# Kernel tuning notes

Measured on AMD Instinct MI355X. Metric: run time of the kernel, lower is better.

## Reference

```python
import jax, jax.numpy as jnp
import numpy as np

GROUP = 4
SG = 4          # shared_gp
C = 256         # inchannels
N = 1024
BS = 16         # GROUP * batch
EPS = 1e-6


def _ln(x, g, b):
    # torch LayerNorm over last dim, biased variance, eps=1e-6
    mu = jnp.mean(x, axis=-1, keepdims=True)
    var = jnp.var(x, axis=-1, keepdims=True)
    return (x - mu) / jnp.sqrt(var + EPS) * g + b


def setup_inputs() -> dict:
    key = jax.random.key(0)
    ks = jax.random.split(key, 12)
    cg = C // SG
    s_conv = 1.0 / np.sqrt(cg)
    s_full = 1.0 / np.sqrt(C)
    return {
        "x": jax.random.normal(ks[0], (BS, C, N), jnp.float32),
        # grouped 1x1 convs (bias=False): weight (SG, C/SG out, C/SG in)
        "Wq": jax.random.normal(ks[1], (SG, cg, cg), jnp.float32) * s_conv,
        "Wk": jax.random.normal(ks[2], (SG, cg, cg), jnp.float32) * s_conv,
        # v conv: full 1x1 conv with bias
        "Wv": jax.random.normal(ks[3], (C, C), jnp.float32) * s_full,
        "bv": jax.random.normal(ks[4], (C,), jnp.float32) * 0.01,
        "ln1_g": jnp.ones((C,), jnp.float32),
        "ln1_b": jnp.zeros((C,), jnp.float32),
        "W1": jax.random.normal(ks[5], (4 * C, C), jnp.float32) * s_full,
        "b1": jax.random.normal(ks[6], (4 * C,), jnp.float32) * 0.01,
        "W2": jax.random.normal(ks[7], (C, 4 * C), jnp.float32) * (1.0 / np.sqrt(4 * C)),
        "b2": jax.random.normal(ks[8], (C,), jnp.float32) * 0.01,
        "ln2_g": jnp.ones((C,), jnp.float32),
        "ln2_b": jnp.zeros((C,), jnp.float32),
    }


def reference(x, Wq, Wk, Wv, bv, ln1_g, ln1_b, W1, b1, W2, b2, ln2_g, ln2_b):
    bs, ch, n = x.shape
    group, sg = GROUP, SG
    b = bs // group
    cg = ch // sg
    first = x[:b]          # (b, C, N)
    last = x[b:]           # ((g-1)*b, C, N)

    # grouped 1x1 convs: y[.,g,o,n] = sum_i W[g,o,i] * x[.,g,i,n]
    xq = jnp.einsum('goi,Bgin->Bgon', Wq, last.reshape((group - 1) * b, sg, cg, n))
    xq = xq.reshape(group - 1, b, sg, cg, n)              # (g-1, b, sg, cg, N)
    xk = jnp.einsum('goi,bgin->bgon', Wk, first.reshape(b, sg, cg, n))  # (b, sg, cg, N)
    xv = jnp.einsum('oc,bcn->bon', Wv, first) + bv[None, :, None]        # (b, C, N)

    # energy: q^T k per shared group, summed over shared groups -> (g-1, b, N, N)
    energy = jnp.einsum('gbscn,bscm->gbnm', xq, xk)
    attn = jax.nn.softmax(energy, axis=-1)
    # x_r[g,b,c,m] = sum_n v[b,c,n] attn[g,b,n,m], scaled by 1/sqrt(C)
    x_r = jnp.einsum('bcn,gbnm->gbcm', xv, attn) / jnp.sqrt(jnp.float32(ch))

    # faithful to torch: vstack (group-major) then view(batch, group-1, ...).mean(1)
    x_r = x_r.reshape(b, group - 1, ch, n).mean(axis=1)   # (b, C, N)

    h = _ln((first + x_r).transpose(0, 2, 1), ln1_g, ln1_b)  # (b, N, C)
    h = h + jax.nn.relu(h @ W1.T + b1) @ W2.T + b2
    h = jax.nn.relu(_ln(h, ln2_g, ln2_b))
    out_first = h.transpose(0, 2, 1)                       # (b, C, N)
    return jnp.concatenate([out_first, last], axis=0)
```

## Files before the change

kernel.cpp:

```cpp
#include <hip/hip_runtime.h>

#define CC 256
#define NN 1024
#define CN (CC*NN)

typedef __attribute__((ext_vector_type(8))) short short8;
typedef __attribute__((ext_vector_type(8))) unsigned short u16x8;
typedef __attribute__((ext_vector_type(4))) float f32x4;

__device__ __forceinline__ unsigned short f2bf(float x) {
  unsigned u = __float_as_uint(x);
  u = u + 0x7fffu + ((u >> 16) & 1u);
  return (unsigned short)(u >> 16);
}
__device__ __forceinline__ float bf2f(unsigned short b) {
  return __uint_as_float(((unsigned)b) << 16);
}
__device__ __forceinline__ void gload_lds16(const unsigned short* g, unsigned short* l) {
  __builtin_amdgcn_global_load_lds(
      (const __attribute__((address_space(1))) unsigned short*)g,
      (__attribute__((address_space(3))) unsigned short*)l, 16, 0, 0);
}

__global__ __launch_bounds__(256) void prep_kernel(
    const float* __restrict__ x, const float* __restrict__ Wq,
    const float* __restrict__ Wk, const float4* __restrict__ Wv,
    const float4* __restrict__ W1, const float4* __restrict__ W2,
    unsigned short* __restrict__ wv_bf, unsigned short* __restrict__ w1_bf,
    unsigned short* __restrict__ w2_bf, unsigned short* __restrict__ xT,
    unsigned short* __restrict__ xqT, unsigned short* __restrict__ xkT) {
  __shared__ float shbuf[64 * 133];
  int bz = blockIdx.x, t = threadIdx.x;
  if (bz < 576) {
    int id = bz * 256 + t;
    const float4* s; unsigned short* d; int k;
    if (id < 16384)      { s = Wv; d = wv_bf; k = id; }
    else if (id < 81920) { s = W1; d = w1_bf; k = id - 16384; }
    else                 { s = W2; d = w2_bf; k = id - 81920; }
    float4 v = s[k];
    ushort4 o; o.x = f2bf(v.x); o.y = f2bf(v.y); o.z = f2bf(v.z); o.w = f2bf(v.w);
    *(ushort4*)&d[k * 4] = o;
  } else if (bz < 832) {
    float (*tile)[65] = (float(*)[65])shbuf;
    int zz = bz - 576;
    int b = zz >> 6, c0 = ((zz >> 4) & 3) * 64, n0 = (zz & 15) * 64;
    int tr = t >> 6, tc = t & 63;
#pragma unroll
    for (int r = 0; r < 16; ++r) {
      int c = tr + r * 4;
      tile[c][tc] = x[(long)b * CN + (long)(c0 + c) * NN + n0 + tc];
    }
    __syncthreads();
#pragma unroll
    for (int r = 0; r < 16; ++r) {
      int n = tr + r * 4;
      xT[(long)b * CN + (long)(n0 + n) * CC + c0 + tc] = f2bf(tile[tc][n]);
    }
  } else {
    float (*xs)[68] = (float(*)[68])shbuf;
    float (*Ws)[65] = (float(*)[65])(shbuf + 64 * 68);
    int zz = bz - 832;
    int z = zz >> 6, g = (zz >> 4) & 3, n0 = (zz & 15) * 64;
    const float* src; const float* W; unsigned short* dst;
    if (z < 12) { src = x + (long)(4 + z) * CN; W = Wq; dst = xqT + (long)z * CN; }
    else        { src = x + (long)(z - 12) * CN; W = Wk; dst = xkT + (long)(z - 12) * CN; }
    int tr = t >> 6, tc = t & 63;
#pragma unroll
    for (int r = 0; r < 16; ++r) {
      int i = tr + r * 4;
      xs[i][tc] = src[(long)(g * 64 + i) * NN + n0 + tc];
      Ws[i][tc] = W[(g * 64 + i) * 64 + tc];
    }
    __syncthreads();
    int o = tc, q = tr;
    float acc[16];
#pragma unroll
    for (int k = 0; k < 16; ++k) acc[k] = 0.f;
    for (int i = 0; i < 64; ++i) {
      float w = Ws[o][i];
      const float4* xr4 = (const float4*)&xs[i][q * 16];
#pragma unroll
      for (int k = 0; k < 4; ++k) {
        float4 v = xr4[k];
        acc[4*k+0] += w * v.x; acc[4*k+1] += w * v.y;
        acc[4*k+2] += w * v.z; acc[4*k+3] += w * v.w;
      }
    }
#pragma unroll
    for (int k = 0; k < 16; ++k)
      dst[(long)(n0 + q * 16 + k) * CC + g * 64 + o] = f2bf(acc[k]);
  }
}

template<int BIASROW, int BIASCOL, int RELU, int RES, int OUTBF, int STATS>
__global__ __launch_bounds__(256) void mgemm(
    const unsigned short* __restrict__ A, const unsigned short* __restrict__ B,
    void* __restrict__ Cout, const float* __restrict__ bias,
    const float* __restrict__ res, float2* __restrict__ part,
    int lda, int ldb, int ldc, int K,
    long sA, int amod, long sB, int bmod, long sC, long sR, float alpha) {
  __shared__ unsigned short As[128 * 32];
  __shared__ unsigned short Bs[128 * 32];
  int z = blockIdx.z;
  A += (long)(z % amod) * sA;
  B += (long)(z % bmod) * sB;
  int t = threadIdx.x, w = t >> 6, l = t & 63;
  int wr = w >> 1, wc = w & 1;
  long i0 = blockIdx.y * 128, j0 = blockIdx.x * 128;
  f32x4 acc[4][4];
#pragma unroll
  for (int a = 0; a < 4; ++a)
#pragma unroll
    for (int b = 0; b < 4; ++b) acc[a][b] = (f32x4){0.f, 0.f, 0.f, 0.f};
  int lr = l & 15, lk = (l >> 4) * 8;
  for (int k0 = 0; k0 < K; k0 += 32) {
#pragma unroll
    for (int it = 0; it < 2; ++it) {
      int chunk = t + it * 256;
      int row = chunk >> 2, kq = chunk & 3;
      gload_lds16(A + (i0 + row) * (long)lda + k0 + kq * 8, &As[chunk * 8]);
      gload_lds16(B + (j0 + row) * (long)ldb + k0 + kq * 8, &Bs[chunk * 8]);
    }
    __syncthreads();
    short8 af[4], bfr[4];
#pragma unroll
    for (int f = 0; f < 4; ++f) af[f]  = *(const short8*)&As[(wr * 64 + f * 16 + lr) * 32 + lk];
#pragma unroll
    for (int f = 0; f < 4; ++f) bfr[f] = *(const short8*)&Bs[(wc * 64 + f * 16 + lr) * 32 + lk];
#pragma unroll
    for (int fm = 0; fm < 4; ++fm)
#pragma unroll
      for (int fn = 0; fn < 4; ++fn)
        acc[fm][fn] = __builtin_amdgcn_mfma_f32_16x16x32_bf16(af[fm], bfr[fn], acc[fm][fn], 0, 0, 0);
    __syncthreads();
  }
  long cz = (long)z * sC;
  long rz = (long)z * sR;
  int li = (l >> 4) * 4, lj = l & 15;
#pragma unroll
  for (int fm = 0; fm < 4; ++fm)
#pragma unroll
    for (int fn = 0; fn < 4; ++fn) {
      long ib = i0 + wr * 64 + fm * 16 + li;
      long j  = j0 + wc * 64 + fn * 16 + lj;
#pragma unroll
      for (int r = 0; r < 4; ++r) {
        long i = ib + r;
        float v = acc[fm][fn][r] * alpha;
        if (BIASCOL) v += bias[j];
        if (BIASROW) v += bias[i];
        if (RES)     v += res[rz + i * ldc + j];
        if (RELU)    v = fmaxf(v, 0.f);
        if (OUTBF) ((unsigned short*)Cout)[cz + i * ldc + j] = f2bf(v);
        else       ((float*)Cout)[cz + i * ldc + j] = v;
      }
    }
  if (STATS) {
    int chunk = blockIdx.y * 2 + wr;
#pragma unroll
    for (int fn = 0; fn < 4; ++fn) {
      float mx = -1e30f;
#pragma unroll
      for (int fm = 0; fm < 4; ++fm)
#pragma unroll
        for (int r = 0; r < 4; ++r) mx = fmaxf(mx, acc[fm][fn][r]);
      mx = fmaxf(mx, __shfl_xor(mx, 16));
      mx = fmaxf(mx, __shfl_xor(mx, 32));
      float sm = 0.f;
#pragma unroll
      for (int fm = 0; fm < 4; ++fm)
#pragma unroll
        for (int r = 0; r < 4; ++r) sm += __expf(acc[fm][fn][r] - mx);
      sm += __shfl_xor(sm, 16);
      sm += __shfl_xor(sm, 32);
      if (l < 16) {
        long n = j0 + wc * 64 + fn * 16 + l;
        part[((long)z * 16 + chunk) * NN + n] = make_float2(mx, sm);
      }
    }
  }
}

__global__ __launch_bounds__(256) void pv_gemm(
    const unsigned short* __restrict__ E, const unsigned short* __restrict__ XV,
    const float2* __restrict__ part, float* __restrict__ xrp) {
  __shared__ unsigned short As[128 * 32];
  __shared__ unsigned short Bs[128 * 32];
  __shared__ float Ms[256];
  __shared__ float Ds[256];
  int z = blockIdx.z;
  int q = z >> 2, s = z & 3;
  const unsigned short* A = E + (long)q * NN * NN + s * 256;
  const unsigned short* B = XV + (long)(q & 3) * CN + s * 256;
  int t = threadIdx.x;
  {
    int n = s * 256 + t;
    float mx = -1e30f;
#pragma unroll
    for (int c = 0; c < 16; ++c) mx = fmaxf(mx, part[((long)q * 16 + c) * NN + n].x);
    float sm = 0.f;
#pragma unroll
    for (int c = 0; c < 16; ++c) {
      float2 p = part[((long)q * 16 + c) * NN + n];
      sm += p.y * __expf(p.x - mx);
    }
    Ms[t] = mx;
    Ds[t] = 1.f / sm;
  }
  int w = t >> 6, l = t & 63;
  int wr = w >> 1, wc = w & 1;
  long i0 = blockIdx.y * 128, j0 = blockIdx.x * 128;
  f32x4 acc[4][4];
#pragma unroll
  for (int a = 0; a < 4; ++a)
#pragma unroll
    for (int b = 0; b < 4; ++b) acc[a][b] = (f32x4){0.f, 0.f, 0.f, 0.f};
  int lr = l & 15, lk = (l >> 4) * 8;
  int ar = t >> 1, ah = (t & 1) * 16;
  __syncthreads();
  for (int k0 = 0; k0 < 256; k0 += 32) {
#pragma unroll
    for (int it = 0; it < 2; ++it) {
      int chunk = t + it * 256;
      int row = chunk >> 2, kq = chunk & 3;
      gload_lds16(B + (j0 + row) * 1024L + k0 + kq * 8, &Bs[chunk * 8]);
    }
    u16x8 e0 = *(const u16x8*)&A[(i0 + ar) * 1024L + k0 + ah];
    u16x8 e1 = *(const u16x8*)&A[(i0 + ar) * 1024L + k0 + ah + 8];
    u16x8 p0, p1;
#pragma unroll
    for (int j = 0; j < 8; ++j) {
      int n = k0 + ah + j;
      p0[j] = f2bf(__expf(bf2f(e0[j]) - Ms[n]) * Ds[n]);
    }
#pragma unroll
    for (int j = 0; j < 8; ++j) {
      int n = k0 + ah + 8 + j;
      p1[j] = f2bf(__expf(bf2f(e1[j]) - Ms[n]) * Ds[n]);
    }
    *(u16x8*)&As[ar * 32 + ah]     = p0;
    *(u16x8*)&As[ar * 32 + ah + 8] = p1;
    __syncthreads();
    short8 af[4], bfr[4];
#pragma unroll
    for (int f = 0; f < 4; ++f) af[f]  = *(const short8*)&As[(wr * 64 + f * 16 + lr) * 32 + lk];
#pragma unroll
    for (int f = 0; f < 4; ++f) bfr[f] = *(const short8*)&Bs[(wc * 64 + f * 16 + lr) * 32 + lk];
#pragma unroll
    for (int fm = 0; fm < 4; ++fm)
#pragma unroll
      for (int fn = 0; fn < 4; ++fn)
        acc[fm][fn] = __builtin_amdgcn_mfma_f32_16x16x32_bf16(af[fm], bfr[fn], acc[fm][fn], 0, 0, 0);
    __syncthreads();
  }
  long cz = (long)(s * 12 + q) << 18;
  int li = (l >> 4) * 4, lj = l & 15;
#pragma unroll
  for (int fm = 0; fm < 4; ++fm)
#pragma unroll
    for (int fn = 0; fn < 4; ++fn) {
      long ib = i0 + wr * 64 + fm * 16 + li;
      long j  = j0 + wc * 64 + fn * 16 + lj;
#pragma unroll
      for (int r = 0; r < 4; ++r)
        xrp[cz + (ib + r) * 256 + j] = acc[fm][fn][r] * (1.f / 16.f);
    }
}

__global__ __launch_bounds__(256) void mix_ln1(
    const unsigned short* __restrict__ xT, const float* __restrict__ xrp,
    const float* __restrict__ g, const float* __restrict__ bb,
    float* __restrict__ h, unsigned short* __restrict__ h_bf) {
  __shared__ float r1[4], r2[4];
  int bn = blockIdx.x;
  int i = bn >> 10, n = bn & 1023;
  int c = threadIdx.x;
  long no = (long)n * CC + c;
  float a = 0.f;
#pragma unroll
  for (int j = 0; j < 3; ++j)
#pragma unroll
    for (int s = 0; s < 4; ++s)
      a += xrp[((long)(s * 12 + 3 * i + j) << 18) + no];
  float v = bf2f(xT[(long)i * CN + no]) + a * (1.f / 3.f);
  float sS = v, s2 = v * v;
#pragma unroll
  for (int m = 32; m; m >>= 1) { sS += __shfl_xor(sS, m); s2 += __shfl_xor(s2, m); }
  if ((c & 63) == 0) { r1[c >> 6] = sS; r2[c >> 6] = s2; }
  __syncthreads();
  float mu = (r1[0] + r1[1] + r1[2] + r1[3]) * (1.f / 256.f);
  float var = (r2[0] + r2[1] + r2[2] + r2[3]) * (1.f / 256.f) - mu * mu;
  float o = (v - mu) * rsqrtf(var + 1e-6f) * g[c] + bb[c];
  h[(long)bn * CC + c] = o;
  h_bf[(long)bn * CC + c] = f2bf(o);
}

__global__ __launch_bounds__(256) void ln2t(
    const float* __restrict__ pm, const float* __restrict__ h,
    const float* __restrict__ b2, const float* __restrict__ g,
    const float* __restrict__ bb, float* __restrict__ out) {
  __shared__ float tile[16][261];
  __shared__ float smu[16], srs[16];
  int i = blockIdx.y, n0 = blockIdx.x * 16;
  int t = threadIdx.x;
  float bc = b2[t];
#pragma unroll
  for (int r = 0; r < 16; ++r) {
    long row = (long)i * NN + n0 + r;
    float v = bc + h[row * CC + t];
#pragma unroll
    for (int s = 0; s < 4; ++s) v += pm[((long)s << 20) + row * CC + t];
    tile[r][t] = v;
  }
  __syncthreads();
  int w = t >> 6, l = t & 63;
#pragma unroll
  for (int rr = 0; rr < 4; ++rr) {
    int r = w * 4 + rr;
    float s = 0.f, s2 = 0.f;
#pragma unroll
    for (int k = 0; k < 4; ++k) { float v = tile[r][l + 64 * k]; s += v; s2 += v * v; }
#pragma unroll
    for (int m = 32; m; m >>= 1) { s += __shfl_xor(s, m); s2 += __shfl_xor(s2, m); }
    if (l == 0) {
      float mu = s * (1.f / 256.f);
      float var = s2 * (1.f / 256.f) - mu * mu;
      smu[r] = mu; srs[r] = rsqrtf(var + 1e-6f);
    }
  }
  __syncthreads();
#pragma unroll
  for (int k = 0; k < 16; ++k) {
    int nn = t & 15, c = (t >> 4) + 16 * k;
    float v = (tile[nn][c] - smu[nn]) * srs[nn] * g[c] + bb[c];
    out[((long)i * CC + c) * NN + n0 + nn] = fmaxf(v, 0.f);
  }
}

extern "C" void kernel_launch(void* const* d_in, const int* in_sizes, int n_in,
                              void* d_out, int out_size, void* d_ws, size_t ws_size,
                              hipStream_t stream) {
  const float* x   = (const float*)d_in[0];
  const float* Wq  = (const float*)d_in[1];
  const float* Wk  = (const float*)d_in[2];
  const float* Wv  = (const float*)d_in[3];
  const float* bv  = (const float*)d_in[4];
  const float* g1  = (const float*)d_in[5];
  const float* b1v = (const float*)d_in[6];
  const float* W1  = (const float*)d_in[7];
  const float* b1m = (const float*)d_in[8];
  const float* W2  = (const float*)d_in[9];
  const float* b2m = (const float*)d_in[10];
  const float* g2  = (const float*)d_in[11];
  const float* b2v = (const float*)d_in[12];
  float* out = (float*)d_out;

  char* base = (char*)d_ws;
  unsigned short* E_bf   = (unsigned short*)base;
  float*          h      = (float*)base;
  unsigned short* h_bf   = (unsigned short*)(base + (4u << 20));
  unsigned short* hid_bf = (unsigned short*)(base + (6u << 20));
  size_t off = 24u << 20;
  float* xrp             = (float*)(base + off);          off += 50331648;
  float* p_mlp           = (float*)(base + off);          off += 16777216;
  unsigned short* wv_bf  = (unsigned short*)(base + off); off += 131072;
  unsigned short* w1_bf  = (unsigned short*)(base + off); off += 524288;
  unsigned short* w2_bf  = (unsigned short*)(base + off); off += 524288;
  unsigned short* xt_bf  = (unsigned short*)(base + off); off += 2097152;
  unsigned short* xqt_bf = (unsigned short*)(base + off); off += 6291456;
  unsigned short* xkt_bf = (unsigned short*)(base + off); off += 2097152;
  unsigned short* xv_bf  = (unsigned short*)(base + off); off += 2097152;
  float2* part           = (float2*)(base + off);         off += 1572864;

  prep_kernel<<<1856, 256, 0, stream>>>(x, Wq, Wk, (const float4*)Wv,
      (const float4*)W1, (const float4*)W2, wv_bf, w1_bf, w2_bf,
      xt_bf, xqt_bf, xkt_bf);
  mgemm<1,0,0,0,1,0><<<dim3(8, 2, 4), 256, 0, stream>>>(
      wv_bf, xt_bf, xv_bf, bv, nullptr, nullptr,
      256, 256, 1024, 256, 0L, 1, (long)CN, 4, (long)CN, 0L, 1.f);
  mgemm<0,0,0,0,1,1><<<dim3(8, 8, 12), 256, 0, stream>>>(
      xkt_bf, xqt_bf, E_bf, nullptr, nullptr, part,
      256, 256, 1024, 256, (long)CN, 4, (long)CN, 12, (long)NN * NN, 0L, 1.f);
  pv_gemm<<<dim3(2, 8, 48), 256, 0, stream>>>(E_bf, xv_bf, part, xrp);
  mix_ln1<<<4096, 256, 0, stream>>>(xt_bf, xrp, g1, b1v, h, h_bf);
  mgemm<0,1,1,0,1,0><<<dim3(8, 32, 1), 256, 0, stream>>>(
      h_bf, w1_bf, hid_bf, b1m, nullptr, nullptr,
      256, 256, 1024, 256, 0L, 1, 0L, 1, 0L, 0L, 1.f);
  mgemm<0,0,0,0,0,0><<<dim3(2, 32, 4), 256, 0, stream>>>(
      hid_bf, w2_bf, p_mlp, nullptr, nullptr, nullptr,
      1024, 1024, 256, 256, 256L, 4, 256L, 4, 1048576L, 0L, 1.f);
  ln2t<<<dim3(64, 4), 256, 0, stream>>>(p_mlp, h, b2m, g2, b2v, out);
  hipMemcpyAsync(out + 4L * CN, x + 4L * CN, 12L * CN * sizeof(float),
                 hipMemcpyDeviceToDevice, stream);
}
```

Baseline: 195.9 us.

## Fuse V projection and passthrough copy into prep, store intermediates in bf16

Computes the V projection in fp32 inside the prep kernel instead of a separate bf16 MFMA GEMM launch. The passthrough copy of the last 12 batches also moves into prep, replacing hipMemcpyAsync. The pv partials, MLP partials and the residual h are now stored in bf16 rather than fp32, and the fp32 h buffer is dropped. This roughly halves intermediate memory traffic and removes two launches, at the cost of extra bf16 rounding error in the residual and the partial sums.

```diff
diff --git a/kernel.cpp b/kernel.cpp
--- a/kernel.cpp
+++ b/kernel.cpp
@@ -24,25 +24,26 @@
 
 __global__ __launch_bounds__(256) void prep_kernel(
     const float* __restrict__ x, const float* __restrict__ Wq,
-    const float* __restrict__ Wk, const float4* __restrict__ Wv,
+    const float* __restrict__ Wk, const float* __restrict__ Wv,
+    const float* __restrict__ bv,
     const float4* __restrict__ W1, const float4* __restrict__ W2,
-    unsigned short* __restrict__ wv_bf, unsigned short* __restrict__ w1_bf,
-    unsigned short* __restrict__ w2_bf, unsigned short* __restrict__ xT,
-    unsigned short* __restrict__ xqT, unsigned short* __restrict__ xkT) {
+    unsigned short* __restrict__ w1_bf, unsigned short* __restrict__ w2_bf,
+    unsigned short* __restrict__ xT, unsigned short* __restrict__ xqT,
+    unsigned short* __restrict__ xkT, unsigned short* __restrict__ xv_bf,
+    float* __restrict__ out) {
   __shared__ float shbuf[64 * 133];
   int bz = blockIdx.x, t = threadIdx.x;
-  if (bz < 576) {
+  if (bz < 512) {
     int id = bz * 256 + t;
     const float4* s; unsigned short* d; int k;
-    if (id < 16384)      { s = Wv; d = wv_bf; k = id; }
-    else if (id < 81920) { s = W1; d = w1_bf; k = id - 16384; }
-    else                 { s = W2; d = w2_bf; k = id - 81920; }
+    if (id < 65536) { s = W1; d = w1_bf; k = id; }
+    else            { s = W2; d = w2_bf; k = id - 65536; }
     float4 v = s[k];
     ushort4 o; o.x = f2bf(v.x); o.y = f2bf(v.y); o.z = f2bf(v.z); o.w = f2bf(v.w);
     *(ushort4*)&d[k * 4] = o;
-  } else if (bz < 832) {
+  } else if (bz < 768) {
     float (*tile)[65] = (float(*)[65])shbuf;
-    int zz = bz - 576;
+    int zz = bz - 512;
     int b = zz >> 6, c0 = ((zz >> 4) & 3) * 64, n0 = (zz & 15) * 64;
     int tr = t >> 6, tc = t & 63;
 #pragma unroll
@@ -56,10 +57,10 @@
       int n = tr + r * 4;
       xT[(long)b * CN + (long)(n0 + n) * CC + c0 + tc] = f2bf(tile[tc][n]);
     }
-  } else {
+  } else if (bz < 1792) {
     float (*xs)[68] = (float(*)[68])shbuf;
     float (*Ws)[65] = (float(*)[65])(shbuf + 64 * 68);
-    int zz = bz - 832;
+    int zz = bz - 768;
     int z = zz >> 6, g = (zz >> 4) & 3, n0 = (zz & 15) * 64;
     const float* src; const float* W; unsigned short* dst;
     if (z < 12) { src = x + (long)(4 + z) * CN; W = Wq; dst = xqT + (long)z * CN; }
@@ -89,16 +90,58 @@
 #pragma unroll
     for (int k = 0; k < 16; ++k)
       dst[(long)(n0 + q * 16 + k) * CC + g * 64 + o] = f2bf(acc[k]);
-  }
-}
-
-template<int BIASROW, int BIASCOL, int RELU, int RES, int OUTBF, int STATS>
+  } else if (bz < 2048) {
+    float (*xs)[68] = (float(*)[68])shbuf;
+    float (*Ws)[65] = (float(*)[65])(shbuf + 64 * 68);
+    int zz = bz - 1792;
+    int b = zz >> 6, o0 = ((zz >> 4) & 3) * 64, n0 = (zz & 15) * 64;
+    int tr = t >> 6, tc = t & 63;
+    float acc[16];
+#pragma unroll
+    for (int k = 0; k < 16; ++k) acc[k] = 0.f;
+    for (int cb = 0; cb < 4; ++cb) {
+      __syncthreads();
+#pragma unroll
+      for (int r = 0; r < 16; ++r) {
+        int i = tr + r * 4;
+        xs[i][tc] = x[(long)b * CN + (long)(cb * 64 + i) * NN + n0 + tc];
+        Ws[i][tc] = Wv[(long)(o0 + i) * 256 + cb * 64 + tc];
+      }
+      __syncthreads();
+      for (int i = 0; i < 64; ++i) {
+        float w = Ws[tc][i];
+        const float4* xr4 = (const float4*)&xs[i][tr * 16];
+#pragma unroll
+        for (int k = 0; k < 4; ++k) {
+          float4 v = xr4[k];
+          acc[4*k+0] += w * v.x; acc[4*k+1] += w * v.y;
+          acc[4*k+2] += w * v.z; acc[4*k+3] += w * v.w;
+        }
+      }
+    }
+    float bvv = bv[o0 + tc];
+#pragma unroll
+    for (int k = 0; k < 16; ++k)
+      xv_bf[((long)b * CC + o0 + tc) * NN + n0 + tr * 16 + k] = f2bf(acc[k] + bvv);
+  } else {
+    int zz = bz - 2048;
+    const float4* src = (const float4*)(x + 4L * CN);
+    float4* dst = (float4*)(out + 4L * CN);
+#pragma unroll
+    for (int k = 0; k < 4; ++k) {
+      int idx = zz * 1024 + k * 256 + t;
+      dst[idx] = src[idx];
+    }
+  }
+}
+
+template<int BIASROW, int BIASCOL, int RELU, int OUTBF, int STATS>
 __global__ __launch_bounds__(256) void mgemm(
     const unsigned short* __restrict__ A, const unsigned short* __restrict__ B,
     void* __restrict__ Cout, const float* __restrict__ bias,
-    const float* __restrict__ res, float2* __restrict__ part,
+    float2* __restrict__ part,
     int lda, int ldb, int ldc, int K,
-    long sA, int amod, long sB, int bmod, long sC, long sR, float alpha) {
+    long sA, int amod, long sB, int bmod, long sC, float alpha) {
   __shared__ unsigned short As[128 * 32];
   __shared__ unsigned short Bs[128 * 32];
   int z = blockIdx.z;
@@ -135,7 +178,6 @@
     __syncthreads();
   }
   long cz = (long)z * sC;
-  long rz = (long)z * sR;
   int li = (l >> 4) * 4, lj = l & 15;
 #pragma unroll
   for (int fm = 0; fm < 4; ++fm)
@@ -149,7 +191,6 @@
         float v = acc[fm][fn][r] * alpha;
         if (BIASCOL) v += bias[j];
         if (BIASROW) v += bias[i];
-        if (RES)     v += res[rz + i * ldc + j];
         if (RELU)    v = fmaxf(v, 0.f);
         if (OUTBF) ((unsigned short*)Cout)[cz + i * ldc + j] = f2bf(v);
         else       ((float*)Cout)[cz + i * ldc + j] = v;
@@ -183,7 +224,7 @@
 
 __global__ __launch_bounds__(256) void pv_gemm(
     const unsigned short* __restrict__ E, const unsigned short* __restrict__ XV,
-    const float2* __restrict__ part, float* __restrict__ xrp) {
+    const float2* __restrict__ part, unsigned short* __restrict__ xrp) {
   __shared__ unsigned short As[128 * 32];
   __shared__ unsigned short Bs[128 * 32];
   __shared__ float Ms[256];
@@ -263,14 +304,14 @@
       long j  = j0 + wc * 64 + fn * 16 + lj;
 #pragma unroll
       for (int r = 0; r < 4; ++r)
-        xrp[cz + (ib + r) * 256 + j] = acc[fm][fn][r] * (1.f / 16.f);
+        xrp[cz + (ib + r) * 256 + j] = f2bf(acc[fm][fn][r] * (1.f / 16.f));
     }
 }
 
 __global__ __launch_bounds__(256) void mix_ln1(
-    const unsigned short* __restrict__ xT, const float* __restrict__ xrp,
+    const unsigned short* __restrict__ xT, const unsigned short* __restrict__ xrp,
     const float* __restrict__ g, const float* __restrict__ bb,
-    float* __restrict__ h, unsigned short* __restrict__ h_bf) {
+    unsigned short* __restrict__ h_bf) {
   __shared__ float r1[4], r2[4];
   int bn = blockIdx.x;
   int i = bn >> 10, n = bn & 1023;
@@ -281,7 +322,7 @@
   for (int j = 0; j < 3; ++j)
 #pragma unroll
     for (int s = 0; s < 4; ++s)
-      a += xrp[((long)(s * 12 + 3 * i + j) << 18) + no];
+      a += bf2f(xrp[((long)(s * 12 + 3 * i + j) << 18) + no]);
   float v = bf2f(xT[(long)i * CN + no]) + a * (1.f / 3.f);
   float sS = v, s2 = v * v;
 #pragma unroll
@@ -291,12 +332,11 @@
   float mu = (r1[0] + r1[1] + r1[2] + r1[3]) * (1.f / 256.f);
   float var = (r2[0] + r2[1] + r2[2] + r2[3]) * (1.f / 256.f) - mu * mu;
   float o = (v - mu) * rsqrtf(var + 1e-6f) * g[c] + bb[c];
-  h[(long)bn * CC + c] = o;
   h_bf[(long)bn * CC + c] = f2bf(o);
 }
 
 __global__ __launch_bounds__(256) void ln2t(
-    const float* __restrict__ pm, const float* __restrict__ h,
+    const unsigned short* __restrict__ pm, const unsigned short* __restrict__ h_bf,
     const float* __restrict__ b2, const float* __restrict__ g,
     const float* __restrict__ bb, float* __restrict__ out) {
   __shared__ float tile[16][261];
@@ -307,9 +347,9 @@
 #pragma unroll
   for (int r = 0; r < 16; ++r) {
     long row = (long)i * NN + n0 + r;
-    float v = bc + h[row * CC + t];
-#pragma unroll
-    for (int s = 0; s < 4; ++s) v += pm[((long)s << 20) + row * CC + t];
+    float v = bc + bf2f(h_bf[row * CC + t]);
+#pragma unroll
+    for (int s = 0; s < 4; ++s) v += bf2f(pm[((long)s << 20) + row * CC + t]);
     tile[r][t] = v;
   }
   __syncthreads();
@@ -357,13 +397,11 @@
 
   char* base = (char*)d_ws;
   unsigned short* E_bf   = (unsigned short*)base;
-  float*          h      = (float*)base;
-  unsigned short* h_bf   = (unsigned short*)(base + (4u << 20));
-  unsigned short* hid_bf = (unsigned short*)(base + (6u << 20));
+  unsigned short* h_bf   = (unsigned short*)base;
+  unsigned short* hid_bf = (unsigned short*)(base + (2u << 20));
   size_t off = 24u << 20;
-  float* xrp             = (float*)(base + off);          off += 50331648;
-  float* p_mlp           = (float*)(base + off);          off += 16777216;
-  unsigned short* wv_bf  = (unsigned short*)(base + off); off += 131072;
+  unsigned short* xrp    = (unsigned short*)(base + off); off += 25165824;
+  unsigned short* p_mlp  = (unsigned short*)(base + off); off += 8388608;
   unsigned short* w1_bf  = (unsigned short*)(base + off); off += 524288;
   unsigned short* w2_bf  = (unsigned short*)(base + off); off += 524288;
   unsigned short* xt_bf  = (unsigned short*)(base + off); off += 2097152;
@@ -372,24 +410,19 @@
   unsigned short* xv_bf  = (unsigned short*)(base + off); off += 2097152;
   float2* part           = (float2*)(base + off);         off += 1572864;
 
-  prep_kernel<<<1856, 256, 0, stream>>>(x, Wq, Wk, (const float4*)Wv,
-      (const float4*)W1, (const float4*)W2, wv_bf, w1_bf, w2_bf,
-      xt_bf, xqt_bf, xkt_bf);
-  mgemm<1,0,0,0,1,0><<<dim3(8, 2, 4), 256, 0, stream>>>(
-      wv_bf, xt_bf, xv_bf, bv, nullptr, nullptr,
-      256, 256, 1024, 256, 0L, 1, (long)CN, 4, (long)CN, 0L, 1.f);
-  mgemm<0,0,0,0,1,1><<<dim3(8, 8, 12), 256, 0, stream>>>(
-      xkt_bf, xqt_bf, E_bf, nullptr, nullptr, part,
-      256, 256, 1024, 256, (long)CN, 4, (long)CN, 12, (long)NN * NN, 0L, 1.f);
+  prep_kernel<<<2816, 256, 0, stream>>>(x, Wq, Wk, Wv, bv,
+      (const float4*)W1, (const float4*)W2, w1_bf, w2_bf,
+      xt_bf, xqt_bf, xkt_bf, xv_bf, out);
+  mgemm<0,0,0,1,1><<<dim3(8, 8, 12), 256, 0, stream>>>(
+      xkt_bf, xqt_bf, E_bf, nullptr, part,
+      256, 256, 1024, 256, (long)CN, 4, (long)CN, 12, (long)NN * NN, 1.f);
   pv_gemm<<<dim3(2, 8, 48), 256, 0, stream>>>(E_bf, xv_bf, part, xrp);
-  mix_ln1<<<4096, 256, 0, stream>>>(xt_bf, xrp, g1, b1v, h, h_bf);
-  mgemm<0,1,1,0,1,0><<<dim3(8, 32, 1), 256, 0, stream>>>(
-      h_bf, w1_bf, hid_bf, b1m, nullptr, nullptr,
-      256, 256, 1024, 256, 0L, 1, 0L, 1, 0L, 0L, 1.f);
-  mgemm<0,0,0,0,0,0><<<dim3(2, 32, 4), 256, 0, stream>>>(
-      hid_bf, w2_bf, p_mlp, nullptr, nullptr, nullptr,
-      1024, 1024, 256, 256, 256L, 4, 256L, 4, 1048576L, 0L, 1.f);
-  ln2t<<<dim3(64, 4), 256, 0, stream>>>(p_mlp, h, b2m, g2, b2v, out);
-  hipMemcpyAsync(out + 4L * CN, x + 4L * CN, 12L * CN * sizeof(float),
-                 hipMemcpyDeviceToDevice, stream);
-}
+  mix_ln1<<<4096, 256, 0, stream>>>(xt_bf, xrp, g1, b1v, h_bf);
+  mgemm<0,1,1,1,0><<<dim3(8, 32, 1), 256, 0, stream>>>(
+      h_bf, w1_bf, hid_bf, b1m, nullptr,
+      256, 256, 1024, 256, 0L, 1, 0L, 1, 0L, 1.f);
+  mgemm<0,0,0,1,0><<<dim3(2, 32, 4), 256, 0, stream>>>(
+      hid_bf, w2_bf, p_mlp, nullptr, nullptr,
+      1024, 1024, 256, 256, 256L, 4, 256L, 4, 1048576L, 1.f);
+  ln2t<<<dim3(64, 4), 256, 0, stream>>>(p_mlp, h_bf, b2m, g2, b2v, out);
+}
```

Result: slower. 200.6 us (+2.4%).
